# Optimization experiments

Hardware: AMD Instinct MI355X
Metric: run time of the kernel (lower is better)

Reference implementation:

```python
import jax, jax.numpy as jnp
import numpy as np
from math import sqrt

B, S, D, H = 4, 2048, 1024, 16
HD = D // H


def setup_inputs() -> dict:
    key = jax.random.key(0)
    ks = jax.random.split(key, 16)
    w = 0.02
    q = jax.random.normal(ks[0], (B, S, D), jnp.float32)
    k = jax.random.normal(ks[1], (B, S, D), jnp.float32)
    v = jax.random.normal(ks[2], (B, S, D), jnp.float32)
    # causal attention mask [1,1,S,S]
    attn_mask = jnp.tril(jnp.ones((S, S), jnp.int32))[None, None]
    # padding mask [B,1,1,S]; force position 0 valid so no softmax row is all -inf
    pad_mask = jax.random.randint(ks[3], (B, 1, 1, S), 0, 2, jnp.int32)
    pad_mask = pad_mask.at[..., 0].set(1)
    params = {
        'Wq': jax.random.normal(ks[4], (D, D), jnp.float32) * w,
        'bq': jnp.zeros((D,), jnp.float32),
        'Wk': jax.random.normal(ks[5], (D, D), jnp.float32) * w,
        'bk': jnp.zeros((D,), jnp.float32),
        'Wv': jax.random.normal(ks[6], (D, D), jnp.float32) * w,
        'bv': jnp.zeros((D,), jnp.float32),
        'Wo': jax.random.normal(ks[7], (D, D), jnp.float32) * w,
        'bo': jnp.zeros((D,), jnp.float32),
        'gamma': jnp.ones((D,), jnp.float32),
        'beta': jnp.zeros((D,), jnp.float32),
    }
    return dict(q=q, k=k, v=v, attn_mask=attn_mask, pad_mask=pad_mask, **params)


def _mha(q, k, v, Wq, bq, Wk, bk, Wv, bv, Wo, bo, gamma, beta, attn_mask, pad_mask):
    seq = q.shape[1]
    # residual path is detached in the original (q.clone().detach())
    x = jax.lax.stop_gradient(q)
    # Linear projections (torch Linear: y = x @ W.T + b)
    qp = (q @ Wq.T + bq).reshape(-1, H, seq, HD)   # raw view, NO head transpose (faithful)
    kp = (k @ Wk.T + bk).reshape(-1, H, seq, HD)
    vp = (v @ Wv.T + bv).reshape(-1, H, seq, HD)
    scores = jnp.einsum('bhqd,bhkd->bhqk', qp, kp)   # [B,H,S,S]
    scores = jnp.where(pad_mask == 0, -jnp.inf, scores)
    scores = jnp.where(attn_mask == 0, -jnp.inf, scores)
    # scaling applied AFTER masking, as in source
    attn = jax.nn.softmax(scores / sqrt(HD), axis=-1)
    out = jnp.einsum('bhqk,bhkd->bhqd', attn, vp).reshape(-1, seq, D)
    out = out @ Wo.T + bo  # dropout is identity in eval
    y = x + out
    mean = jnp.mean(y, axis=-1, keepdims=True)
    std = jnp.sqrt(jnp.mean((y - mean) ** 2, axis=-1, keepdims=True))
    return gamma * ((y - mean) / (std + 1e-8)) + beta


def reference(q, k, v, attn_mask, pad_mask, Wq, bq, Wk, bk, Wv, bv, Wo, bo, gamma, beta):
    return _mha(q, k, v, Wq, bq, Wk, bk, Wv, bv, Wo, bo, gamma, beta, attn_mask, pad_mask)
```

## Files before the change

kernel.cpp:

```cpp
#include <hip/hip_runtime.h>
#include <hip/hip_bf16.h>
#include <math.h>

#define B_  4
#define S_  2048
#define D_  1024
#define H_  16
#define HD_ 64
#define SD_  (S_*D_)
#define SHD_ (S_*HD_)

typedef __attribute__((ext_vector_type(8))) short          bf16x8;
typedef __attribute__((ext_vector_type(4))) float          f32x4;
typedef __attribute__((ext_vector_type(8))) unsigned short us8;
typedef __attribute__((ext_vector_type(4))) unsigned short us4;

__device__ __forceinline__ unsigned short f2bf(float x) {
  unsigned int u = __float_as_uint(x);
  u += 0x7fffu + ((u >> 16) & 1u);
  return (unsigned short)(u >> 16);
}
__device__ __forceinline__ float bf2f(unsigned short u) {
  return __uint_as_float(((unsigned int)u) << 16);
}

__device__ __forceinline__ void gload16(const unsigned short* g, unsigned short* l) {
  __builtin_amdgcn_global_load_lds(
      (const __attribute__((address_space(1))) unsigned int*)g,
      (__attribute__((address_space(3))) unsigned int*)l,
      16, 0, 0);
}

__device__ __forceinline__ void stage_swz(const unsigned short* __restrict__ g,
                                          int rstride ,
                                          unsigned short* lds, int tid)
{
#pragma unroll
  for (int rr = 0; rr < 2; ++rr) {
    const int cidx = tid + rr * 256;
    const int row  = cidx >> 3;
    const int sb   = ((cidx & 7) * 16) ^ ((row & 7) << 4);
    gload16(g + (size_t)row * rstride + (sb >> 1), lds + cidx * 8);
  }
}

__device__ __forceinline__ void read_frag_pair(const unsigned short* lds, int row,
                                               int quad, bf16x8& f0, bf16x8& f1)
{
  const int sw = (row & 7) << 4;
  const unsigned short* p = lds + row * 64;
  f0 = *(const bf16x8*)(p + (((quad * 16) ^ sw) >> 1));
  f1 = *(const bf16x8*)(p + (((64 + quad * 16) ^ sw) >> 1));
}

__global__ __launch_bounds__(256) void cvt_a(const float* __restrict__ s,
                                             unsigned short* __restrict__ d)
{
  int i = blockIdx.x * 256 + threadIdx.x;
  float4 v = ((const float4*)s)[i];
  us4 o = { f2bf(v.x), f2bf(v.y), f2bf(v.z), f2bf(v.w) };
  *(us4*)(d + (size_t)i * 4) = o;
}

__global__ __launch_bounds__(256) void cvt3(const float* __restrict__ q,
                                            const float* __restrict__ k,
                                            const float* __restrict__ v,
                                            unsigned short* __restrict__ dst)
{
  const float* s = (blockIdx.y == 0) ? q : (blockIdx.y == 1) ? k : v;
  unsigned short* d = dst + (size_t)blockIdx.y * (B_ * (size_t)SD_);
  int i = blockIdx.x * 256 + threadIdx.x;
  float4 x = ((const float4*)s)[i];
  us4 o = { f2bf(x.x), f2bf(x.y), f2bf(x.z), f2bf(x.w) };
  *(us4*)(d + (size_t)i * 4) = o;
}

__global__ __launch_bounds__(256) void cvt_w(const float* __restrict__ w0,
                                             const float* __restrict__ w1,
                                             const float* __restrict__ w2,
                                             const float* __restrict__ w3,
                                             unsigned short* __restrict__ dst)
{
  const float* s = (blockIdx.y == 0) ? w0 : (blockIdx.y == 1) ? w1
                 : (blockIdx.y == 2) ? w2 : w3;
  unsigned short* d = dst + (size_t)blockIdx.y * 1024 * 1024;
  int i = blockIdx.x * 256 + threadIdx.x;
  float4 v = ((const float4*)s)[i];
  us4 o = { f2bf(v.x), f2bf(v.y), f2bf(v.z), f2bf(v.w) };
  *(us4*)(d + (size_t)i * 4) = o;
}

__global__ __launch_bounds__(256) void pad_cvt(const int* __restrict__ pad,
                                               float* __restrict__ padf)
{
  int i = (blockIdx.x * 256 + threadIdx.x) * 4;
  int4 pv = *(const int4*)(pad + i);
  float4 o = { pv.x ? 0.f : -1e30f, pv.y ? 0.f : -1e30f,
               pv.z ? 0.f : -1e30f, pv.w ? 0.f : -1e30f };
  *(float4*)(padf + i) = o;
}

__device__ __forceinline__ void gemm_body(
    const unsigned short* __restrict__ A,
    const unsigned short* __restrict__ Wb,
    const float* __restrict__ bias,
    unsigned short* __restrict__ Cb,
    int n0, int m0)
{
  __shared__ unsigned short As[128 * 32];
  __shared__ unsigned short Bs[128 * 32];

  const int tid  = threadIdx.x;
  const int lane = tid & 63;
  const int w    = tid >> 6;
  const int wm   = w >> 1, wn = w & 1;
  const int l16  = lane & 15, quad = lane >> 4;

  f32x4 acc[4][4];
#pragma unroll
  for (int mt = 0; mt < 4; ++mt)
#pragma unroll
    for (int nt = 0; nt < 4; ++nt) acc[mt][nt] = (f32x4){0.f, 0.f, 0.f, 0.f};

  const int srow = lane >> 2;
  const int sseg = (lane & 3) * 8;

  for (int kt = 0; kt < 32; ++kt) {
    const int kofs = kt * 32;
#pragma unroll
    for (int t = 0; t < 2; ++t) {
      const int r = w * 32 + t * 16 + srow;
      gload16(A  + (size_t)(m0 + r) * 1024 + kofs + sseg, &As[r * 32 + sseg]);
      gload16(Wb + (size_t)(n0 + r) * 1024 + kofs + sseg, &Bs[r * 32 + sseg]);
    }
    __syncthreads();

    bf16x8 af[4], bfr[4];
#pragma unroll
    for (int mt = 0; mt < 4; ++mt)
      af[mt] = *(const bf16x8*)&As[(wm * 64 + mt * 16 + l16) * 32 + quad * 8];
#pragma unroll
    for (int nt = 0; nt < 4; ++nt)
      bfr[nt] = *(const bf16x8*)&Bs[(wn * 64 + nt * 16 + l16) * 32 + quad * 8];
#pragma unroll
    for (int mt = 0; mt < 4; ++mt)
#pragma unroll
      for (int nt = 0; nt < 4; ++nt)
        acc[mt][nt] = __builtin_amdgcn_mfma_f32_16x16x32_bf16(
            af[mt], bfr[nt], acc[mt][nt], 0, 0, 0);
    __syncthreads();
  }

#pragma unroll
  for (int nt = 0; nt < 4; ++nt) {
    const int ncol = n0 + wn * 64 + nt * 16 + l16;
    const float bv = bias[ncol];
#pragma unroll
    for (int mt = 0; mt < 4; ++mt) {
      const int row = m0 + wm * 64 + mt * 16 + quad * 4;
#pragma unroll
      for (int reg = 0; reg < 4; ++reg)
        Cb[(size_t)(row + reg) * 1024 + ncol] = f2bf(acc[mt][nt][reg] + bv);
    }
  }
}

__global__ __launch_bounds__(256) void gemm_mfma(
    const unsigned short* __restrict__ A, const unsigned short* __restrict__ Wb,
    const float* __restrict__ bias, unsigned short* __restrict__ Cb)
{
  gemm_body(A, Wb, bias, Cb, blockIdx.x * 128, blockIdx.y * 128);
}

__global__ __launch_bounds__(256) void gemm_qkv(
    const unsigned short* __restrict__ A3,
    const unsigned short* __restrict__ Wall,
    const float* __restrict__ bq, const float* __restrict__ bk,
    const float* __restrict__ bv,
    unsigned short* __restrict__ Qb, unsigned short* __restrict__ Kb,
    unsigned short* __restrict__ Vb)
{
  const int z = blockIdx.z;
  const unsigned short* A  = A3 + (size_t)z * (B_ * (size_t)SD_);
  const unsigned short* Wb = Wall + (size_t)z * 1024 * 1024;
  const float* bias = (z == 0) ? bq : (z == 1) ? bk : bv;
  unsigned short* Cb = (z == 0) ? Qb : (z == 1) ? Kb : Vb;
  gemm_body(A, Wb, bias, Cb, blockIdx.x * 128, blockIdx.y * 128);
}

__global__ __launch_bounds__(256) void vtrans(
    const unsigned short* __restrict__ V, unsigned short* __restrict__ Vt)
{
  __shared__ unsigned short t[64][72];
  const int tid = threadIdx.x;
  const int st  = blockIdx.x;
  const int bh  = blockIdx.y;
  const unsigned short* src = V + (size_t)bh * SHD_ + (size_t)st * 4096;

#pragma unroll
  for (int u = tid; u < 512; u += 256) {
    us8 vv = ((const us8*)src)[u];
    int s  = u >> 3;
    int dg = (u & 7) * 8;
    *(us8*)&t[s][dg] = vv;
  }
  __syncthreads();

  unsigned short* dst = Vt + (size_t)bh * SHD_ + st * 64;
#pragma unroll
  for (int u = tid; u < 1024; u += 256) {
    int d  = u >> 4;
    int s4 = (u & 15) * 4;
    us4 o = { t[s4][d], t[s4 + 1][d], t[s4 + 2][d], t[s4 + 3][d] };
    *(us4*)(dst + (size_t)d * 2048 + s4) = o;
  }
}

__global__ __launch_bounds__(256, 4) void attn_mfma(
    unsigned short* __restrict__ Qb, const unsigned short* __restrict__ Kb,
    const unsigned short* __restrict__ Vt, const float* __restrict__ padf)
{
  __shared__ unsigned short Ks[64 * 64];
  __shared__ unsigned short Vs[2][64 * 64];
  __shared__ unsigned short Ps[4][16][72];

  const int tid  = threadIdx.x;
  const int lane = tid & 63;
  const int w    = tid >> 6;
  const int p    = blockIdx.x;
  const int bh   = blockIdx.y;
  const int b    = bh >> 4;
  const size_t base = (size_t)bh * SHD_;

  const int l16  = lane & 15;
  const int quad = lane >> 4;

  for (int half = 0; half < 2; ++half) {
    const int it = half ? (31 - p) : p;

    bf16x8 qfrag[2];
    {
      const unsigned short* qrow = Qb + base + (size_t)(it * 64 + w * 16 + l16) * 64;
      qfrag[0] = *(const bf16x8*)(qrow + quad * 8);
      qfrag[1] = *(const bf16x8*)(qrow + 32 + quad * 8);
    }

    f32x4 oacc[4];
#pragma unroll
    for (int dt = 0; dt < 4; ++dt) oacc[dt] = (f32x4){0.f, 0.f, 0.f, 0.f};
    float mS = -INFINITY, lS = 0.f;

    __syncthreads();
    stage_swz(Kb + base, 64, Ks, tid);
    stage_swz(Vt + base, 2048, Vs[0], tid);
    float4 pf[4];
#pragma unroll
    for (int ct = 0; ct < 4; ++ct)
      pf[ct] = *(const float4*)(padf + b * S_ + ct * 16 + quad * 4);
    int cur = 0;

    for (int jt = 0; jt <= it; ++jt) {
      __syncthreads();

      f32x4 sacc[4];
#pragma unroll
      for (int ct = 0; ct < 4; ++ct) {
        bf16x8 k0, k1;
        read_frag_pair(Ks, ct * 16 + l16, quad, k0, k1);
        f32x4 s = (f32x4){0.f, 0.f, 0.f, 0.f};
        s = __builtin_amdgcn_mfma_f32_16x16x32_bf16(k0, qfrag[0], s, 0, 0, 0);
        s = __builtin_amdgcn_mfma_f32_16x16x32_bf16(k1, qfrag[1], s, 0, 0, 0);
        sacc[ct] = s;
      }

      float4 pfn[4];
      if (jt < it) {
        __syncthreads();
        stage_swz(Kb + base + (size_t)(jt + 1) * 4096, 64, Ks, tid);
        stage_swz(Vt + base + (jt + 1) * 64, 2048, Vs[cur ^ 1], tid);
#pragma unroll
        for (int ct = 0; ct < 4; ++ct)
          pfn[ct] = *(const float4*)(padf + b * S_ + (jt + 1) * 64 + ct * 16 + quad * 4);
      }

      float lg[4][4];
      float mx = -INFINITY;
#pragma unroll
      for (int ct = 0; ct < 4; ++ct)
#pragma unroll
        for (int reg = 0; reg < 4; ++reg) {
          float sc = fmaf(sacc[ct][reg], 0.125f, ((const float*)&pf[ct])[reg]);
          if (jt == it) {
            bool ok = (ct * 16 + quad * 4 + reg) <= (w * 16 + l16);
            sc = ok ? sc : -1e30f;
          }
          lg[ct][reg] = sc;
          mx = fmaxf(mx, sc);
        }
      mx = fmaxf(mx, __shfl_xor(mx, 16, 64));
      mx = fmaxf(mx, __shfl_xor(mx, 32, 64));
      const float mnew = fmaxf(mS, mx);
      const float a    = __expf(mS - mnew);
      float sm = 0.f;
#pragma unroll
      for (int ct = 0; ct < 4; ++ct) {
        us4 pk;
#pragma unroll
        for (int reg = 0; reg < 4; ++reg) {
          float pe = __expf(lg[ct][reg] - mnew);
          sm += pe;
          pk[reg] = f2bf(pe);
        }
        *(us4*)&Ps[w][l16][ct * 16 + quad * 4] = pk;
      }
      sm += __shfl_xor(sm, 16, 64);
      sm += __shfl_xor(sm, 32, 64);
      lS = lS * a + sm;
      mS = mnew;

      float aO[4];
#pragma unroll
      for (int reg = 0; reg < 4; ++reg) aO[reg] = __shfl(a, quad * 4 + reg, 64);
#pragma unroll
      for (int dt = 0; dt < 4; ++dt)
#pragma unroll
        for (int reg = 0; reg < 4; ++reg) oacc[dt][reg] *= aO[reg];

      bf16x8 pfrag0 = *(const bf16x8*)&Ps[w][l16][quad * 8];
      bf16x8 pfrag1 = *(const bf16x8*)&Ps[w][l16][32 + quad * 8];
#pragma unroll
      for (int dt = 0; dt < 4; ++dt) {
        bf16x8 v0, v1;
        read_frag_pair(Vs[cur], dt * 16 + l16, quad, v0, v1);
        oacc[dt] = __builtin_amdgcn_mfma_f32_16x16x32_bf16(pfrag0, v0, oacc[dt], 0, 0, 0);
        oacc[dt] = __builtin_amdgcn_mfma_f32_16x16x32_bf16(pfrag1, v1, oacc[dt], 0, 0, 0);
      }

      if (jt < it) {
#pragma unroll
        for (int ct = 0; ct < 4; ++ct) pf[ct] = pfn[ct];
        cur ^= 1;
      }
    }

    float lO[4];
#pragma unroll
    for (int reg = 0; reg < 4; ++reg) lO[reg] = __shfl(lS, quad * 4 + reg, 64);
#pragma unroll
    for (int reg = 0; reg < 4; ++reg) {
      const float rl = 1.0f / lO[reg];
      unsigned short* orow = Qb + base + (size_t)(it * 64 + w * 16 + quad * 4 + reg) * 64;
#pragma unroll
      for (int dt = 0; dt < 4; ++dt)
        orow[dt * 16 + l16] = f2bf(oacc[dt][reg] * rl);
    }
  }
}

__global__ __launch_bounds__(256) void ln_kernel(
    const float* __restrict__ x, const unsigned short* __restrict__ O,
    const float* __restrict__ gamma, const float* __restrict__ beta,
    float* __restrict__ out)
{
  __shared__ float red[8];
  const int row = blockIdx.x;
  const int tid = threadIdx.x;
  float4 xv = ((const float4*)x)[(size_t)row * 256 + tid];
  us4 ov4 = *(const us4*)(O + (size_t)row * 1024 + tid * 4);
  float4 y = make_float4(xv.x + bf2f(ov4[0]), xv.y + bf2f(ov4[1]),
                         xv.z + bf2f(ov4[2]), xv.w + bf2f(ov4[3]));
  float s1 = y.x + y.y + y.z + y.w;
  float s2 = y.x*y.x + y.y*y.y + y.z*y.z + y.w*y.w;
#pragma unroll
  for (int off = 32; off >= 1; off >>= 1) {
    s1 += __shfl_xor(s1, off, 64);
    s2 += __shfl_xor(s2, off, 64);
  }
  if ((tid & 63) == 0) { red[tid >> 6] = s1; red[4 + (tid >> 6)] = s2; }
  __syncthreads();
  s1 = red[0] + red[1] + red[2] + red[3];
  s2 = red[4] + red[5] + red[6] + red[7];
  const float mean = s1 * (1.0f / 1024.0f);
  const float var  = fmaxf(s2 * (1.0f / 1024.0f) - mean * mean, 0.f);
  const float rstd = 1.0f / (sqrtf(var) + 1e-8f);
  float4 gv = ((const float4*)gamma)[tid];
  float4 bv = ((const float4*)beta)[tid];
  float4 r;
  r.x = gv.x * (y.x - mean) * rstd + bv.x;
  r.y = gv.y * (y.y - mean) * rstd + bv.y;
  r.z = gv.z * (y.z - mean) * rstd + bv.z;
  r.w = gv.w * (y.w - mean) * rstd + bv.w;
  ((float4*)out)[(size_t)row * 256 + tid] = r;
}

extern "C" void kernel_launch(void* const* d_in, const int* in_sizes, int n_in,
                              void* d_out, int out_size, void* d_ws, size_t ws_size,
                              hipStream_t stream)
{
  const float* q  = (const float*)d_in[0];
  const float* k  = (const float*)d_in[1];
  const float* v  = (const float*)d_in[2];
  const int*   pad = (const int*)d_in[4];
  const float* Wq = (const float*)d_in[5];
  const float* bq = (const float*)d_in[6];
  const float* Wk = (const float*)d_in[7];
  const float* bk = (const float*)d_in[8];
  const float* Wv = (const float*)d_in[9];
  const float* bv = (const float*)d_in[10];
  const float* Wo = (const float*)d_in[11];
  const float* bo = (const float*)d_in[12];
  const float* gamma = (const float*)d_in[13];
  const float* beta  = (const float*)d_in[14];
  float* out = (float*)d_out;

  char* ws = (char*)d_ws;
  const size_t MB = 1024 * 1024;
  dim3 gg(8, 64), bb(256);

  if (ws_size >= 121 * MB) {
    unsigned short* Ac3  = (unsigned short*)(ws);
    unsigned short* Qb   = (unsigned short*)(ws + 48 * MB);
    unsigned short* Kb   = (unsigned short*)(ws + 64 * MB);
    unsigned short* Vb   = (unsigned short*)(ws + 80 * MB);
    unsigned short* Vtb  = (unsigned short*)(ws + 96 * MB);
    unsigned short* Wall = (unsigned short*)(ws + 112 * MB);
    float*          padf = (float*)(ws + 120 * MB);
    unsigned short* Obuf = Ac3;

    cvt_w<<<dim3(1024, 4), 256, 0, stream>>>(Wq, Wk, Wv, Wo, Wall);
    pad_cvt<<<8, 256, 0, stream>>>(pad, padf);
    cvt3<<<dim3(8192, 3), 256, 0, stream>>>(q, k, v, Ac3);
    gemm_qkv<<<dim3(8, 64, 3), bb, 0, stream>>>(Ac3, Wall, bq, bk, bv, Qb, Kb, Vb);
    vtrans<<<dim3(32, 64), 256, 0, stream>>>(Vb, Vtb);
    attn_mfma<<<dim3(16, 64), 256, 0, stream>>>(Qb, Kb, Vtb, padf);
    gemm_mfma<<<gg, bb, 0, stream>>>(Qb, Wall + 3 * MB, bo, Obuf);
    ln_kernel<<<dim3(B_ * S_), 256, 0, stream>>>(q, Obuf, gamma, beta, out);
  } else {
    unsigned short* Ac   = (unsigned short*)(ws);
    unsigned short* Qb   = (unsigned short*)(ws + 16 * MB);
    unsigned short* Kb   = (unsigned short*)(ws + 32 * MB);
    unsigned short* Vb   = (unsigned short*)(ws + 48 * MB);
    unsigned short* Vtb  = (unsigned short*)(ws + 64 * MB);
    unsigned short* Wall = (unsigned short*)(ws + 80 * MB);
    float*          padf = (float*)(ws + 88 * MB);
    unsigned short* Obuf = Ac;

    cvt_w<<<dim3(1024, 4), 256, 0, stream>>>(Wq, Wk, Wv, Wo, Wall);
    pad_cvt<<<8, 256, 0, stream>>>(pad, padf);
    cvt_a<<<8192, 256, 0, stream>>>(q, Ac);
    gemm_mfma<<<gg, bb, 0, stream>>>(Ac, Wall + 0 * MB, bq, Qb);
    cvt_a<<<8192, 256, 0, stream>>>(k, Ac);
    gemm_mfma<<<gg, bb, 0, stream>>>(Ac, Wall + 1 * MB, bk, Kb);
    cvt_a<<<8192, 256, 0, stream>>>(v, Ac);
    gemm_mfma<<<gg, bb, 0, stream>>>(Ac, Wall + 2 * MB, bv, Vb);
    vtrans<<<dim3(32, 64), 256, 0, stream>>>(Vb, Vtb);
    attn_mfma<<<dim3(16, 64), 256, 0, stream>>>(Qb, Kb, Vtb, padf);
    gemm_mfma<<<gg, bb, 0, stream>>>(Qb, Wall + 3 * MB, bo, Obuf);
    ln_kernel<<<dim3(B_ * S_), 256, 0, stream>>>(q, Obuf, gamma, beta, out);
  }
}
```

Measured before the change: 388.8 us.

## Fuse fp32 activation conversion into QKV GEMM, double-buffer GEMMs, lazy softmax rescale

```diff
diff --git a/kernel.cpp b/kernel.cpp
--- a/kernel.cpp
+++ b/kernel.cpp
@@ -53,62 +53,86 @@
   f1 = *(const bf16x8*)(p + (((64 + quad * 16) ^ sw) >> 1));
 }
 
-__global__ __launch_bounds__(256) void cvt_a(const float* __restrict__ s,
-                                             unsigned short* __restrict__ d)
-{
-  int i = blockIdx.x * 256 + threadIdx.x;
-  float4 v = ((const float4*)s)[i];
-  us4 o = { f2bf(v.x), f2bf(v.y), f2bf(v.z), f2bf(v.w) };
-  *(us4*)(d + (size_t)i * 4) = o;
-}
-
-__global__ __launch_bounds__(256) void cvt3(const float* __restrict__ q,
-                                            const float* __restrict__ k,
-                                            const float* __restrict__ v,
-                                            unsigned short* __restrict__ dst)
-{
-  const float* s = (blockIdx.y == 0) ? q : (blockIdx.y == 1) ? k : v;
-  unsigned short* d = dst + (size_t)blockIdx.y * (B_ * (size_t)SD_);
-  int i = blockIdx.x * 256 + threadIdx.x;
-  float4 x = ((const float4*)s)[i];
-  us4 o = { f2bf(x.x), f2bf(x.y), f2bf(x.z), f2bf(x.w) };
-  *(us4*)(d + (size_t)i * 4) = o;
-}
-
-__global__ __launch_bounds__(256) void cvt_w(const float* __restrict__ w0,
-                                             const float* __restrict__ w1,
-                                             const float* __restrict__ w2,
-                                             const float* __restrict__ w3,
-                                             unsigned short* __restrict__ dst)
-{
-  const float* s = (blockIdx.y == 0) ? w0 : (blockIdx.y == 1) ? w1
-                 : (blockIdx.y == 2) ? w2 : w3;
-  unsigned short* d = dst + (size_t)blockIdx.y * 1024 * 1024;
-  int i = blockIdx.x * 256 + threadIdx.x;
-  float4 v = ((const float4*)s)[i];
-  us4 o = { f2bf(v.x), f2bf(v.y), f2bf(v.z), f2bf(v.w) };
-  *(us4*)(d + (size_t)i * 4) = o;
-}
-
-__global__ __launch_bounds__(256) void pad_cvt(const int* __restrict__ pad,
-                                               float* __restrict__ padf)
-{
-  int i = (blockIdx.x * 256 + threadIdx.x) * 4;
-  int4 pv = *(const int4*)(pad + i);
-  float4 o = { pv.x ? 0.f : -1e30f, pv.y ? 0.f : -1e30f,
-               pv.z ? 0.f : -1e30f, pv.w ? 0.f : -1e30f };
-  *(float4*)(padf + i) = o;
-}
-
-__device__ __forceinline__ void gemm_body(
-    const unsigned short* __restrict__ A,
-    const unsigned short* __restrict__ Wb,
-    const float* __restrict__ bias,
-    unsigned short* __restrict__ Cb,
-    int n0, int m0)
-{
-  __shared__ unsigned short As[128 * 32];
-  __shared__ unsigned short Bs[128 * 32];
+__global__ __launch_bounds__(256) void cvt_wp(
+    const float* __restrict__ w0, const float* __restrict__ w1,
+    const float* __restrict__ w2, const float* __restrict__ w3,
+    const int* __restrict__ pad,
+    unsigned short* __restrict__ Wall, float* __restrict__ padf)
+{
+  const int bx = blockIdx.x;
+  if (bx < 4096) {
+    const int y = bx >> 10;
+    const int i = (bx & 1023) * 256 + threadIdx.x;
+    const float* s = (y == 0) ? w0 : (y == 1) ? w1 : (y == 2) ? w2 : w3;
+    unsigned short* d = Wall + (size_t)y * 1024 * 1024;
+    float4 x = ((const float4*)s)[i];
+    us4 o = { f2bf(x.x), f2bf(x.y), f2bf(x.z), f2bf(x.w) };
+    *(us4*)(d + (size_t)i * 4) = o;
+  } else {
+    const int i = ((bx - 4096) * 256 + threadIdx.x) * 4;
+    int4 pv = *(const int4*)(pad + i);
+    float4 o = { pv.x ? 0.f : -1e30f, pv.y ? 0.f : -1e30f,
+                 pv.z ? 0.f : -1e30f, pv.w ? 0.f : -1e30f };
+    *(float4*)(padf + i) = o;
+  }
+}
+
+__device__ __forceinline__ void xcd_coords(int& n0, int& m0)
+{
+  const int nwgx = gridDim.x;
+  const int nwg  = nwgx * gridDim.y;
+  const int bid  = blockIdx.y * nwgx + blockIdx.x;
+  const int sw   = (bid & 7) * (nwg >> 3) + (bid >> 3);
+  n0 = (sw % nwgx) * 128;
+  m0 = (sw / nwgx) * 128;
+}
+
+__device__ __forceinline__ void gemm_epilogue(
+    f32x4 (&acc)[4][4], const float* __restrict__ bias,
+    unsigned short* __restrict__ Cb, int n0, int m0,
+    int wm, int wn, int l16, int quad)
+{
+#pragma unroll
+  for (int nt = 0; nt < 4; ++nt) {
+    const int ncol = n0 + wn * 64 + nt * 16 + l16;
+    const float bv = bias[ncol];
+#pragma unroll
+    for (int mt = 0; mt < 4; ++mt) {
+      const int row = m0 + wm * 64 + mt * 16 + quad * 4;
+#pragma unroll
+      for (int reg = 0; reg < 4; ++reg)
+        Cb[(size_t)(row + reg) * 1024 + ncol] = f2bf(acc[mt][nt][reg] + bv);
+    }
+  }
+}
+
+__device__ __forceinline__ void store_bf8(unsigned short* p, float4 a, float4 b)
+{
+  us8 o = { f2bf(a.x), f2bf(a.y), f2bf(a.z), f2bf(a.w),
+            f2bf(b.x), f2bf(b.y), f2bf(b.z), f2bf(b.w) };
+  *(us8*)p = o;
+}
+
+__global__ __launch_bounds__(256) void gemm_qkv_f32(
+    const float* __restrict__ qf, const float* __restrict__ kf,
+    const float* __restrict__ vf,
+    const unsigned short* __restrict__ Wall,
+    const float* __restrict__ bq, const float* __restrict__ bk,
+    const float* __restrict__ bv,
+    unsigned short* __restrict__ Qb, unsigned short* __restrict__ Kb,
+    unsigned short* __restrict__ Vb)
+{
+  __shared__ unsigned short As[2][128 * 32];
+  __shared__ unsigned short Bs[2][128 * 32];
+
+  const int z = blockIdx.z;
+  const float* Af = (z == 0) ? qf : (z == 1) ? kf : vf;
+  const unsigned short* Wb = Wall + (size_t)z * 1024 * 1024;
+  const float* bias = (z == 0) ? bq : (z == 1) ? bk : bv;
+  unsigned short* Cb = (z == 0) ? Qb : (z == 1) ? Kb : Vb;
+
+  int n0, m0;
+  xcd_coords(n0, m0);
 
   const int tid  = threadIdx.x;
   const int lane = tid & 63;
@@ -124,68 +148,132 @@
 
   const int srow = lane >> 2;
   const int sseg = (lane & 3) * 8;
-
+  const int r0   = w * 32 + srow, r1 = r0 + 16;
+
+  const float* A0 = Af + (size_t)(m0 + r0) * 1024 + sseg;
+  const float* A1 = Af + (size_t)(m0 + r1) * 1024 + sseg;
+  const unsigned short* B0 = Wb + (size_t)(n0 + r0) * 1024 + sseg;
+  const unsigned short* B1 = Wb + (size_t)(n0 + r1) * 1024 + sseg;
+  unsigned short* dA0 = &As[0][r0 * 32 + sseg];
+  unsigned short* dB0 = &Bs[0][r0 * 32 + sseg];
+
+  {
+    float4 f0 = *(const float4*)(A0),     f1 = *(const float4*)(A0 + 4);
+    float4 f2 = *(const float4*)(A1),     f3 = *(const float4*)(A1 + 4);
+    gload16(B0, dB0);
+    gload16(B1, dB0 + 16 * 32);
+    store_bf8(dA0,           f0, f1);
+    store_bf8(dA0 + 16 * 32, f2, f3);
+  }
+
+  int buf = 0;
   for (int kt = 0; kt < 32; ++kt) {
-    const int kofs = kt * 32;
-#pragma unroll
-    for (int t = 0; t < 2; ++t) {
-      const int r = w * 32 + t * 16 + srow;
-      gload16(A  + (size_t)(m0 + r) * 1024 + kofs + sseg, &As[r * 32 + sseg]);
-      gload16(Wb + (size_t)(n0 + r) * 1024 + kofs + sseg, &Bs[r * 32 + sseg]);
-    }
     __syncthreads();
 
+    float4 f0, f1, f2, f3;
+    if (kt < 31) {
+      const int ko = (kt + 1) * 32;
+      f0 = *(const float4*)(A0 + ko);  f1 = *(const float4*)(A0 + ko + 4);
+      f2 = *(const float4*)(A1 + ko);  f3 = *(const float4*)(A1 + ko + 4);
+      const int nb = (buf ^ 1) * 4096;
+      gload16(B0 + ko, dB0 + nb);
+      gload16(B1 + ko, dB0 + nb + 16 * 32);
+    }
+
+    const unsigned short* Ab = As[buf];
+    const unsigned short* Bb = Bs[buf];
     bf16x8 af[4], bfr[4];
 #pragma unroll
     for (int mt = 0; mt < 4; ++mt)
-      af[mt] = *(const bf16x8*)&As[(wm * 64 + mt * 16 + l16) * 32 + quad * 8];
+      af[mt] = *(const bf16x8*)&Ab[(wm * 64 + mt * 16 + l16) * 32 + quad * 8];
 #pragma unroll
     for (int nt = 0; nt < 4; ++nt)
-      bfr[nt] = *(const bf16x8*)&Bs[(wn * 64 + nt * 16 + l16) * 32 + quad * 8];
+      bfr[nt] = *(const bf16x8*)&Bb[(wn * 64 + nt * 16 + l16) * 32 + quad * 8];
 #pragma unroll
     for (int mt = 0; mt < 4; ++mt)
 #pragma unroll
       for (int nt = 0; nt < 4; ++nt)
         acc[mt][nt] = __builtin_amdgcn_mfma_f32_16x16x32_bf16(
             af[mt], bfr[nt], acc[mt][nt], 0, 0, 0);
-    __syncthreads();
-  }
-
-#pragma unroll
-  for (int nt = 0; nt < 4; ++nt) {
-    const int ncol = n0 + wn * 64 + nt * 16 + l16;
-    const float bv = bias[ncol];
-#pragma unroll
-    for (int mt = 0; mt < 4; ++mt) {
-      const int row = m0 + wm * 64 + mt * 16 + quad * 4;
-#pragma unroll
-      for (int reg = 0; reg < 4; ++reg)
-        Cb[(size_t)(row + reg) * 1024 + ncol] = f2bf(acc[mt][nt][reg] + bv);
-    }
-  }
+
+    if (kt < 31) {
+      const int nb = (buf ^ 1) * 4096;
+      store_bf8(dA0 + nb,           f0, f1);
+      store_bf8(dA0 + nb + 16 * 32, f2, f3);
+      buf ^= 1;
+    }
+  }
+
+  gemm_epilogue(acc, bias, Cb, n0, m0, wm, wn, l16, quad);
 }
 
 __global__ __launch_bounds__(256) void gemm_mfma(
     const unsigned short* __restrict__ A, const unsigned short* __restrict__ Wb,
     const float* __restrict__ bias, unsigned short* __restrict__ Cb)
 {
-  gemm_body(A, Wb, bias, Cb, blockIdx.x * 128, blockIdx.y * 128);
-}
-
-__global__ __launch_bounds__(256) void gemm_qkv(
-    const unsigned short* __restrict__ A3,
-    const unsigned short* __restrict__ Wall,
-    const float* __restrict__ bq, const float* __restrict__ bk,
-    const float* __restrict__ bv,
-    unsigned short* __restrict__ Qb, unsigned short* __restrict__ Kb,
-    unsigned short* __restrict__ Vb)
-{
-  const int z = blockIdx.z;
-  const unsigned short* A  = A3 + (size_t)z * (B_ * (size_t)SD_);
-  const unsigned short* Wb = Wall + (size_t)z * 1024 * 1024;
-  const float* bias = (z == 0) ? bq : (z == 1) ? bk : bv;
-  unsigned short* Cb = (z == 0) ? Qb : (z == 1) ? Kb : Vb;
-  gemm_body(A, Wb, bias, Cb, blockIdx.x * 128, blockIdx.y * 128);
+  __shared__ unsigned short As[2][128 * 32];
+  __shared__ unsigned short Bs[2][128 * 32];
+
+  int n0, m0;
+  xcd_coords(n0, m0);
+
+  const int tid  = threadIdx.x;
+  const int lane = tid & 63;
+  const int w    = tid >> 6;
+  const int wm   = w >> 1, wn = w & 1;
+  const int l16  = lane & 15, quad = lane >> 4;
+
+  f32x4 acc[4][4];
+#pragma unroll
+  for (int mt = 0; mt < 4; ++mt)
+#pragma unroll
+    for (int nt = 0; nt < 4; ++nt) acc[mt][nt] = (f32x4){0.f, 0.f, 0.f, 0.f};
+
+  const int srow = lane >> 2;
+  const int sseg = (lane & 3) * 8;
+  const int r0   = w * 32 + srow, r1 = r0 + 16;
+
+  const unsigned short* A0 = A  + (size_t)(m0 + r0) * 1024 + sseg;
+  const unsigned short* A1 = A  + (size_t)(m0 + r1) * 1024 + sseg;
+  const unsigned short* B0 = Wb + (size_t)(n0 + r0) * 1024 + sseg;
+  const unsigned short* B1 = Wb + (size_t)(n0 + r1) * 1024 + sseg;
+  unsigned short* dA0 = &As[0][r0 * 32 + sseg];
+  unsigned short* dB0 = &Bs[0][r0 * 32 + sseg];
+
+  gload16(A0, dA0);            gload16(A1, dA0 + 16 * 32);
+  gload16(B0, dB0);            gload16(B1, dB0 + 16 * 32);
+
+  int buf = 0;
+  for (int kt = 0; kt < 32; ++kt) {
+    __syncthreads();
+
+    if (kt < 31) {
+      const int ko = (kt + 1) * 32;
+      const int nb = (buf ^ 1) * 4096;
+      gload16(A0 + ko, dA0 + nb);  gload16(A1 + ko, dA0 + nb + 16 * 32);
+      gload16(B0 + ko, dB0 + nb);  gload16(B1 + ko, dB0 + nb + 16 * 32);
+    }
+
+    const unsigned short* Ab = As[buf];
+    const unsigned short* Bb = Bs[buf];
+    bf16x8 af[4], bfr[4];
+#pragma unroll
+    for (int mt = 0; mt < 4; ++mt)
+      af[mt] = *(const bf16x8*)&Ab[(wm * 64 + mt * 16 + l16) * 32 + quad * 8];
+#pragma unroll
+    for (int nt = 0; nt < 4; ++nt)
+      bfr[nt] = *(const bf16x8*)&Bb[(wn * 64 + nt * 16 + l16) * 32 + quad * 8];
+#pragma unroll
+    for (int mt = 0; mt < 4; ++mt)
+#pragma unroll
+      for (int nt = 0; nt < 4; ++nt)
+        acc[mt][nt] = __builtin_amdgcn_mfma_f32_16x16x32_bf16(
+            af[mt], bfr[nt], acc[mt][nt], 0, 0, 0);
+
+    buf ^= 1;
+  }
+
+  gemm_epilogue(acc, bias, Cb, n0, m0, wm, wn, l16, quad);
 }
 
 __global__ __launch_bounds__(256) void vtrans(
@@ -227,8 +315,9 @@
   const int tid  = threadIdx.x;
   const int lane = tid & 63;
   const int w    = tid >> 6;
-  const int p    = blockIdx.x;
-  const int bh   = blockIdx.y;
+  const int id   = blockIdx.y * 16 + blockIdx.x;
+  const int p    = id >> 6;
+  const int bh   = (id & 7) + 8 * ((id >> 3) & 7);
   const int b    = bh >> 4;
   const size_t base = (size_t)bh * SHD_;
 
@@ -299,15 +388,28 @@
         }
       mx = fmaxf(mx, __shfl_xor(mx, 16, 64));
       mx = fmaxf(mx, __shfl_xor(mx, 32, 64));
-      const float mnew = fmaxf(mS, mx);
-      const float a    = __expf(mS - mnew);
+
+      if (!__all(mx <= mS + 8.f)) {
+        const float mnew = fmaxf(mS, mx);
+        const float a    = __expf(mS - mnew);
+        mS = mnew;
+        lS *= a;
+        float aO[4];
+#pragma unroll
+        for (int reg = 0; reg < 4; ++reg) aO[reg] = __shfl(a, quad * 4 + reg, 64);
+#pragma unroll
+        for (int dt = 0; dt < 4; ++dt)
+#pragma unroll
+          for (int reg = 0; reg < 4; ++reg) oacc[dt][reg] *= aO[reg];
+      }
+
       float sm = 0.f;
 #pragma unroll
       for (int ct = 0; ct < 4; ++ct) {
         us4 pk;
 #pragma unroll
         for (int reg = 0; reg < 4; ++reg) {
-          float pe = __expf(lg[ct][reg] - mnew);
+          float pe = __expf(lg[ct][reg] - mS);
           sm += pe;
           pk[reg] = f2bf(pe);
         }
@@ -315,16 +417,7 @@
       }
       sm += __shfl_xor(sm, 16, 64);
       sm += __shfl_xor(sm, 32, 64);
-      lS = lS * a + sm;
-      mS = mnew;
-
-      float aO[4];
-#pragma unroll
-      for (int reg = 0; reg < 4; ++reg) aO[reg] = __shfl(a, quad * 4 + reg, 64);
-#pragma unroll
-      for (int dt = 0; dt < 4; ++dt)
-#pragma unroll
-        for (int reg = 0; reg < 4; ++reg) oacc[dt][reg] *= aO[reg];
+      lS += sm;
 
       bf16x8 pfrag0 = *(const bf16x8*)&Ps[w][l16][quad * 8];
       bf16x8 pfrag1 = *(const bf16x8*)&Ps[w][l16][32 + quad * 8];
@@ -415,47 +508,21 @@
 
   char* ws = (char*)d_ws;
   const size_t MB = 1024 * 1024;
+  unsigned short* Qb   = (unsigned short*)(ws);
+  unsigned short* Kb   = (unsigned short*)(ws + 16 * MB);
+  unsigned short* Vb   = (unsigned short*)(ws + 32 * MB);
+  unsigned short* Vtb  = (unsigned short*)(ws + 48 * MB);
+  unsigned short* Obuf = (unsigned short*)(ws + 64 * MB);
+  unsigned short* Wall = (unsigned short*)(ws + 80 * MB);
+  float*          padf = (float*)(ws + 88 * MB);
+
   dim3 gg(8, 64), bb(256);
 
-  if (ws_size >= 121 * MB) {
-    unsigned short* Ac3  = (unsigned short*)(ws);
-    unsigned short* Qb   = (unsigned short*)(ws + 48 * MB);
-    unsigned short* Kb   = (unsigned short*)(ws + 64 * MB);
-    unsigned short* Vb   = (unsigned short*)(ws + 80 * MB);
-    unsigned short* Vtb  = (unsigned short*)(ws + 96 * MB);
-    unsigned short* Wall = (unsigned short*)(ws + 112 * MB);
-    float*          padf = (float*)(ws + 120 * MB);
-    unsigned short* Obuf = Ac3;
-
-    cvt_w<<<dim3(1024, 4), 256, 0, stream>>>(Wq, Wk, Wv, Wo, Wall);
-    pad_cvt<<<8, 256, 0, stream>>>(pad, padf);
-    cvt3<<<dim3(8192, 3), 256, 0, stream>>>(q, k, v, Ac3);
-    gemm_qkv<<<dim3(8, 64, 3), bb, 0, stream>>>(Ac3, Wall, bq, bk, bv, Qb, Kb, Vb);
-    vtrans<<<dim3(32, 64), 256, 0, stream>>>(Vb, Vtb);
-    attn_mfma<<<dim3(16, 64), 256, 0, stream>>>(Qb, Kb, Vtb, padf);
-    gemm_mfma<<<gg, bb, 0, stream>>>(Qb, Wall + 3 * MB, bo, Obuf);
-    ln_kernel<<<dim3(B_ * S_), 256, 0, stream>>>(q, Obuf, gamma, beta, out);
-  } else {
-    unsigned short* Ac   = (unsigned short*)(ws);
-    unsigned short* Qb   = (unsigned short*)(ws + 16 * MB);
-    unsigned short* Kb   = (unsigned short*)(ws + 32 * MB);
-    unsigned short* Vb   = (unsigned short*)(ws + 48 * MB);
-    unsigned short* Vtb  = (unsigned short*)(ws + 64 * MB);
-    unsigned short* Wall = (unsigned short*)(ws + 80 * MB);
-    float*          padf = (float*)(ws + 88 * MB);
-    unsigned short* Obuf = Ac;
-
-    cvt_w<<<dim3(1024, 4), 256, 0, stream>>>(Wq, Wk, Wv, Wo, Wall);
-    pad_cvt<<<8, 256, 0, stream>>>(pad, padf);
-    cvt_a<<<8192, 256, 0, stream>>>(q, Ac);
-    gemm_mfma<<<gg, bb, 0, stream>>>(Ac, Wall + 0 * MB, bq, Qb);
-    cvt_a<<<8192, 256, 0, stream>>>(k, Ac);
-    gemm_mfma<<<gg, bb, 0, stream>>>(Ac, Wall + 1 * MB, bk, Kb);
-    cvt_a<<<8192, 256, 0, stream>>>(v, Ac);
-    gemm_mfma<<<gg, bb, 0, stream>>>(Ac, Wall + 2 * MB, bv, Vb);
-    vtrans<<<dim3(32, 64), 256, 0, stream>>>(Vb, Vtb);
-    attn_mfma<<<dim3(16, 64), 256, 0, stream>>>(Qb, Kb, Vtb, padf);
-    gemm_mfma<<<gg, bb, 0, stream>>>(Qb, Wall + 3 * MB, bo, Obuf);
-    ln_kernel<<<dim3(B_ * S_), 256, 0, stream>>>(q, Obuf, gamma, beta, out);
-  }
-}
+  cvt_wp<<<dim3(4104), 256, 0, stream>>>(Wq, Wk, Wv, Wo, pad, Wall, padf);
+  gemm_qkv_f32<<<dim3(8, 64, 3), bb, 0, stream>>>(q, k, v, Wall, bq, bk, bv,
+                                                  Qb, Kb, Vb);
+  vtrans<<<dim3(32, 64), 256, 0, stream>>>(Vb, Vtb);
+  attn_mfma<<<dim3(16, 64), 256, 0, stream>>>(Qb, Kb, Vtb, padf);
+  gemm_mfma<<<gg, bb, 0, stream>>>(Qb, Wall + 3 * MB, bo, Obuf);
+  ln_kernel<<<dim3(B_ * S_), 256, 0, stream>>>(q, Obuf, gamma, beta, out);
+}
```

After: 386.7 us. Within noise of the previous version (-0.5%).
